# Kernel tuning notes

Hardware: AMD Instinct MI355X
Metric: run time of the kernel (lower is better)

Reference implementation:

```python
import jax, jax.numpy as jnp
import numpy as np

L, B, T, C, H, FC = 8, 4, 2048, 1024, 16, 4
HD = C // H  # head dim = 64
DFF = FC * C  # 4096


def _layernorm(x, g, b, eps=1e-5):
    mu = jnp.mean(x, axis=-1, keepdims=True)
    var = jnp.mean(jnp.square(x - mu), axis=-1, keepdims=True)
    return (x - mu) * jax.lax.rsqrt(var + eps) * g + b


def setup_inputs() -> dict:
    key = jax.random.key(0)
    ks = jax.random.split(key, 18)
    s = 0.02
    d = {}
    d["x"] = jax.random.normal(ks[0], (B, T, C), jnp.float32)
    d["ln1_g"] = jnp.ones((L, C), jnp.float32)
    d["ln1_b"] = jnp.zeros((L, C), jnp.float32)
    d["ln2_g"] = jnp.ones((L, C), jnp.float32)
    d["ln2_b"] = jnp.zeros((L, C), jnp.float32)
    d["wq"] = jax.random.normal(ks[1], (L, C, C), jnp.float32) * s
    d["bq"] = jnp.zeros((L, C), jnp.float32)
    d["wk"] = jax.random.normal(ks[2], (L, C, C), jnp.float32) * s
    d["bk"] = jnp.zeros((L, C), jnp.float32)
    d["wv"] = jax.random.normal(ks[3], (L, C, C), jnp.float32) * s
    d["bv"] = jnp.zeros((L, C), jnp.float32)
    d["wo"] = jax.random.normal(ks[4], (L, C, C), jnp.float32) * s
    d["bo"] = jnp.zeros((L, C), jnp.float32)
    d["w1"] = jax.random.normal(ks[5], (L, C, DFF), jnp.float32) * s
    d["b1"] = jnp.zeros((L, DFF), jnp.float32)
    d["w2"] = jax.random.normal(ks[6], (L, DFF, C), jnp.float32) * s
    d["b2"] = jnp.zeros((L, C), jnp.float32)
    return d


def _forward(x, ln1_g, ln1_b, ln2_g, ln2_b, wq, bq, wk, bk, wv, bv, wo, bo, w1, b1, w2, b2):
    mask = jnp.tril(jnp.ones((T, T), dtype=bool))  # causal mask (block_size buffer)
    scale = 1.0 / np.sqrt(HD).astype(np.float32)

    def block(h, p):
        g1, be1, g2, be2, Wq, Bq, Wk, Bk, Wv, Bv, Wo, Bo, W1, B1, W2, B2 = p
        hn = _layernorm(h, g1, be1)
        # heads: [B, H, T, HD]
        q = (hn @ Wq + Bq).reshape(B, T, H, HD).transpose(0, 2, 1, 3)
        k = (hn @ Wk + Bk).reshape(B, T, H, HD).transpose(0, 2, 1, 3)
        v = (hn @ Wv + Bv).reshape(B, T, H, HD).transpose(0, 2, 1, 3)
        att = jnp.einsum('bhid,bhjd->bhij', q, k) * scale
        att = jnp.where(mask, att, -jnp.inf)
        att = jax.nn.softmax(att, axis=-1)
        y = jnp.einsum('bhij,bhjd->bhid', att, v)
        y = y.transpose(0, 2, 1, 3).reshape(B, T, C) @ Wo + Bo
        h = h + y
        m = _layernorm(h, g2, be2)
        h = h + jax.nn.gelu(m @ W1 + B1, approximate=False) @ W2 + B2
        return h, None

    params = (ln1_g, ln1_b, ln2_g, ln2_b, wq, bq, wk, bk, wv, bv, wo, bo, w1, b1, w2, b2)
    x, _ = jax.lax.scan(block, x, params)
    return x


def reference(x, ln1_g, ln1_b, ln2_g, ln2_b, wq, bq, wk, bk, wv, bv, wo, bo, w1, b1, w2, b2):
    return _forward(x, ln1_g, ln1_b, ln2_g, ln2_b, wq, bq, wk, bk, wv, bv, wo, bo, w1, b1, w2, b2)
```

## Files before the change

kernel.cpp:

```cpp
#include <hip/hip_runtime.h>
#include <hip/hip_bf16.h>

#define LL 8
#define BBx 4
#define TT 2048
#define CC 1024
#define HH 16
#define HDD 64
#define DFFx 4096
#define MMx 8192

typedef __bf16 bf16;
typedef __attribute__((ext_vector_type(8))) __bf16 bf16x8;
typedef __attribute__((ext_vector_type(4))) __bf16 bf16x4;
typedef __attribute__((ext_vector_type(4))) float f32x4;
typedef __attribute__((ext_vector_type(8))) unsigned short u16x8;

__device__ __forceinline__ unsigned short bfbits(float v) {
  return __builtin_bit_cast(unsigned short, (__bf16)v);
}

__device__ __forceinline__ int xcd_swz(int id, int nwg) {
  return (id & 7) * (nwg >> 3) + (id >> 3);
}

#define GLDS(gp, lp) __builtin_amdgcn_global_load_lds( \
    (const __attribute__((address_space(1))) void*)(gp), \
    (__attribute__((address_space(3))) void*)(lp), 16, 0, 0)

__global__ __launch_bounds__(256) void transpose_cast(
    const float* __restrict__ W, bf16* __restrict__ Wt,
    int K, int N, long srcStride, long dstStride)
{
  __shared__ float tile[32][33];
  const float* Wl = W + (size_t)blockIdx.z * srcStride;
  bf16* Wtl = Wt + (size_t)blockIdx.z * dstStride;
  const int n0 = blockIdx.x * 32, k0 = blockIdx.y * 32;
  const int tx = threadIdx.x, ty = threadIdx.y;
#pragma unroll
  for (int i = 0; i < 32; i += 8)
    tile[ty + i][tx] = Wl[(size_t)(k0 + ty + i) * N + n0 + tx];
  __syncthreads();
#pragma unroll
  for (int i = 0; i < 32; i += 8)
    Wtl[(size_t)(n0 + ty + i) * K + k0 + tx] = (bf16)tile[tx][ty + i];
}

__global__ __launch_bounds__(256) void ln_cmb(
    float* __restrict__ h, const float* __restrict__ p0, const float* __restrict__ p1,
    const float* __restrict__ gamma, const float* __restrict__ beta,
    bf16* __restrict__ out)
{
  const int row = blockIdx.x, tid = threadIdx.x;
  const size_t base = (size_t)row * CC + tid * 4;
  float4 v = *(const float4*)(h + base);
  if (p0) {
    const float4 a = *(const float4*)(p0 + base);
    const float4 b = *(const float4*)(p1 + base);
    v.x += a.x + b.x; v.y += a.y + b.y; v.z += a.z + b.z; v.w += a.w + b.w;
    *(float4*)(h + base) = v;
  }
  if (!out) return;
  float s  = v.x + v.y + v.z + v.w;
  float ss = v.x * v.x + v.y * v.y + v.z * v.z + v.w * v.w;
#pragma unroll
  for (int o = 32; o >= 1; o >>= 1) {
    s  += __shfl_xor(s, o);
    ss += __shfl_xor(ss, o);
  }
  __shared__ float rs[4], rss[4];
  const int w = tid >> 6, l = tid & 63;
  if (l == 0) { rs[w] = s; rss[w] = ss; }
  __syncthreads();
  s  = rs[0] + rs[1] + rs[2] + rs[3];
  ss = rss[0] + rss[1] + rss[2] + rss[3];
  const float mu = s * (1.f / CC);
  const float rstd = rsqrtf(ss * (1.f / CC) - mu * mu + 1e-5f);
  const float4 g  = *(const float4*)(gamma + tid * 4);
  const float4 be = *(const float4*)(beta + tid * 4);
  bf16x4 o4;
  o4[0] = (bf16)((v.x - mu) * rstd * g.x + be.x);
  o4[1] = (bf16)((v.y - mu) * rstd * g.y + be.y);
  o4[2] = (bf16)((v.z - mu) * rstd * g.z + be.z);
  o4[3] = (bf16)((v.w - mu) * rstd * g.w + be.w);
  *(bf16x4*)(out + (size_t)row * CC + tid * 4) = o4;
}

template<int EPI>
__global__ __launch_bounds__(512, 2) void gemm256(
    const bf16* __restrict__ A, const bf16* __restrict__ Bt,
    const float* __restrict__ bias0, const float* __restrict__ bias1,
    const float* __restrict__ bias2,
    bf16* __restrict__ o0, bf16* __restrict__ o1, bf16* __restrict__ o2,
    float* __restrict__ p0, float* __restrict__ p1,
    int M, int N, int K, int lda)
{
  __shared__ __align__(16) bf16 sA[2][256 * 64];
  __shared__ __align__(16) bf16 sB[2][256 * 64];
  const int nx = N >> 8;
  int wk = xcd_swz((int)blockIdx.x, (int)gridDim.x);
  int koff = 0;
  float* part = p0;
  bool addb = true;
  if constexpr (EPI == 1) {
    const int tiles = nx * (M >> 8);
    const int ks = wk / tiles;
    wk -= ks * tiles;
    koff = ks * K;
    addb = (ks == 0);
    part = ks ? p1 : p0;
  }
  const int m0 = (wk / nx) * 256;
  const int n0 = (wk % nx) * 256;
  const int tid = threadIdx.x;
  const int w = tid >> 6, l = tid & 63;
  const int wm = w >> 2, wn = w & 3;
  const int lr = l & 15, lk = l >> 4;
  const int sr = tid >> 3, ss = tid & 7;

  f32x4 acc[8][4] = {};
  const int NT = K >> 6;

  auto stage = [&](int b, int kt) {
    const int gc = ((ss ^ (sr & 7)) << 3) + kt * 64 + koff;
#pragma unroll
    for (int i = 0; i < 4; ++i) {
      const int r = sr + i * 64;
      const int dst = r * 64 + ss * 8;
      GLDS(A + (size_t)(m0 + r) * lda + gc, &sA[b][dst]);
      GLDS(Bt + (size_t)(n0 + r) * lda + gc, &sB[b][dst]);
    }
  };

  stage(0, 0);
  int cur = 0;
  for (int kt = 0; kt < NT; ++kt) {
    if (kt + 1 < NT) {
      stage(cur ^ 1, kt + 1);
      asm volatile("s_waitcnt vmcnt(8)" ::: "memory");
    } else {
      asm volatile("s_waitcnt vmcnt(0)" ::: "memory");
    }
    __builtin_amdgcn_s_barrier();
#pragma unroll
    for (int kk = 0; kk < 2; ++kk) {
      bf16x8 af[8], bfr[4];
#pragma unroll
      for (int m = 0; m < 8; ++m) {
        const int row = wm * 128 + m * 16 + lr;
        af[m] = *(const bf16x8*)&sA[cur][row * 64 + (((kk * 4 + lk) ^ (row & 7)) << 3)];
      }
#pragma unroll
      for (int j = 0; j < 4; ++j) {
        const int row = wn * 64 + j * 16 + lr;
        bfr[j] = *(const bf16x8*)&sB[cur][row * 64 + (((kk * 4 + lk) ^ (row & 7)) << 3)];
      }
#pragma unroll
      for (int m = 0; m < 8; ++m)
#pragma unroll
        for (int j = 0; j < 4; ++j)
          acc[m][j] = __builtin_amdgcn_mfma_f32_16x16x32_bf16(af[m], bfr[j], acc[m][j], 0, 0, 0);
    }
    __builtin_amdgcn_s_barrier();
    cur ^= 1;
  }

  if constexpr (EPI == 0) {
    const int seg = n0 >> 10;
    const float* bp = (seg == 0) ? bias0 : (seg == 1 ? bias1 : bias2);
    if (seg < 2) {
      float bv4[4];
#pragma unroll
      for (int j = 0; j < 4; ++j) bv4[j] = bp[(n0 + wn * 64 + j * 16 + lr) & 1023];
      const int hh = ((n0 + wn * 64) & 1023) >> 6;
      bf16* dst = (seg == 0) ? o0 : o1;
#pragma unroll
      for (int m = 0; m < 8; ++m) {
        const int mrow = m0 + wm * 128 + m * 16 + lk * 4;
        const int bidx = mrow >> 11, t = mrow & 2047;
#pragma unroll
        for (int r = 0; r < 4; ++r) {
          bf16* rowp = dst + (((size_t)(bidx * HH + hh)) * TT + t + r) * HDD;
#pragma unroll
          for (int j = 0; j < 4; ++j)
            rowp[j * 16 + lr] = (bf16)(acc[m][j][r] + bv4[j]);
        }
      }
    } else {
      char* scb = (char*)((w < 4) ? (&sA[0][0] + w * 8192) : (&sB[0][0] + (w - 4) * 8192));
#pragma unroll
      for (int j = 0; j < 4; ++j) {
        const int dl = j * 16 + lr;
        const float bv = bias2[(n0 + wn * 64 + dl) & 1023];
#pragma unroll
        for (int m = 0; m < 8; ++m) {
          ushort4 pk;
          pk.x = bfbits(acc[m][j][0] + bv);
          pk.y = bfbits(acc[m][j][1] + bv);
          pk.z = bfbits(acc[m][j][2] + bv);
          pk.w = bfbits(acc[m][j][3] + bv);
          *(ushort4*)(scb + dl * 256 + (((m * 16 + lk * 4) * 2) ^ ((dl & 7) << 4))) = pk;
        }
      }
      asm volatile("s_waitcnt lgkmcnt(0)" ::: "memory");
      const int hh = ((n0 + wn * 64) & 1023) >> 6;
      const int bidx = m0 >> 11;
      const int tb = ((m0 + wm * 128) & 2047);
      const int c = l & 15;
#pragma unroll
      for (int g = 0; g < 16; ++g) {
        const int dl = g * 4 + lk;
        u16x8 val = *(const u16x8*)(scb + dl * 256 + ((c * 16) ^ ((dl & 7) << 4)));
        *(u16x8*)&o2[(((size_t)(bidx * HH + hh)) * HDD + dl) * TT + tb + c * 8] = val;
      }
    }
  } else if constexpr (EPI == 1) {
    float bv4[4];
#pragma unroll
    for (int j = 0; j < 4; ++j)
      bv4[j] = addb ? bias0[n0 + wn * 64 + j * 16 + lr] : 0.f;
#pragma unroll
    for (int m = 0; m < 8; ++m) {
      const int mrow = m0 + wm * 128 + m * 16 + lk * 4;
#pragma unroll
      for (int r = 0; r < 4; ++r) {
        float* rowp = part + (size_t)(mrow + r) * N + n0 + wn * 64;
#pragma unroll
        for (int j = 0; j < 4; ++j)
          rowp[j * 16 + lr] = acc[m][j][r] + bv4[j];
      }
    }
  } else {
    float bv4[4];
#pragma unroll
    for (int j = 0; j < 4; ++j) bv4[j] = bias0[n0 + wn * 64 + j * 16 + lr];
#pragma unroll
    for (int m = 0; m < 8; ++m) {
      const int mrow = m0 + wm * 128 + m * 16 + lk * 4;
#pragma unroll
      for (int r = 0; r < 4; ++r) {
        bf16* rowp = o0 + (size_t)(mrow + r) * N + n0 + wn * 64;
#pragma unroll
        for (int j = 0; j < 4; ++j) {
          const float x = acc[m][j][r] + bv4[j];
          rowp[j * 16 + lr] = (bf16)(0.5f * x * (1.f + erff(x * 0.70710678f)));
        }
      }
    }
  }
  (void)M;
}

__global__ __launch_bounds__(256) void attn_fwd(
    const bf16* __restrict__ Q, const bf16* __restrict__ Kk,
    const bf16* __restrict__ Vt, bf16* __restrict__ O)
{
  const int wk = xcd_swz((int)blockIdx.x, (int)gridDim.x);
  const int bh = wk >> 3;
  const int xt = wk & 7;
  const int tid = threadIdx.x;
  const int w = tid >> 6, l = tid & 63;
  const int lr = l & 15, lk = l >> 4;
  const int bidx = bh >> 4, hh = bh & 15;

  const bf16* Qp = Q  + (size_t)bh * (TT * HDD);
  const bf16* Kp = Kk + (size_t)bh * (TT * HDD);
  const bf16* Vp = Vt + (size_t)bh * (HDD * TT);

  __shared__ __align__(16) bf16 sK[64 * 64];
  __shared__ __align__(16) bf16 sV[64 * 64];
  __shared__ __align__(16) bf16 sP[4][16 * 64];
  bf16* sPw = &sP[w][0];

  const float sc = 0.125f;
  const int swz = (lr & 7) * 8;
  const int srow = tid >> 3;
  const int scol = (((tid & 7) ^ (srow & 7)) << 3);
  const int sdst = tid << 3;

  for (int half = 0; half < 2; ++half) {
    const int qtile = (half == 0) ? xt : (15 - xt);
    const int q0 = qtile * 128;

    bf16x8 qf[2][2];
#pragma unroll
    for (int qi = 0; qi < 2; ++qi)
#pragma unroll
      for (int dk = 0; dk < 2; ++dk)
        qf[qi][dk] = *(const bf16x8*)&Qp[(size_t)(q0 + w * 32 + qi * 16 + lr) * HDD + dk * 32 + lk * 8];

    f32x4 accO[2][4] = {};
    float mrun[2] = {-__builtin_inff(), -__builtin_inff()};
    float lrun[2] = {0.f, 0.f};
    const int wqmax = q0 + w * 32 + 31;
    const int kvend = q0 + 128;

    for (int kv = 0; kv < kvend; kv += 64) {
      __syncthreads();
#pragma unroll
      for (int i = 0; i < 2; ++i) {
        GLDS(Kp + (size_t)(kv + srow + i * 32) * HDD + scol, sK + sdst + i * 2048);
        GLDS(Vp + (size_t)(srow + i * 32) * TT + kv + scol, sV + sdst + i * 2048);
      }
      __syncthreads();

      if (kv <= wqmax) {
#pragma unroll
        for (int qi = 0; qi < 2; ++qi) {
          f32x4 st[4];
#pragma unroll
          for (int kt = 0; kt < 4; ++kt) {
            f32x4 z = {0.f, 0.f, 0.f, 0.f};
#pragma unroll
            for (int dk = 0; dk < 2; ++dk) {
              bf16x8 kf = *(const bf16x8*)&sK[(kt * 16 + lr) * 64 + ((dk * 32 + lk * 8) ^ swz)];
              z = __builtin_amdgcn_mfma_f32_16x16x32_bf16(kf, qf[qi][dk], z, 0, 0, 0);
            }
            st[kt] = z;
          }
          const int qabs = q0 + w * 32 + qi * 16 + lr;
          float pm = -__builtin_inff();
#pragma unroll
          for (int kt = 0; kt < 4; ++kt)
#pragma unroll
            for (int r = 0; r < 4; ++r) {
              const int kvabs = kv + kt * 16 + lk * 4 + r;
              float val = st[kt][r] * sc;
              val = (kvabs > qabs) ? -__builtin_inff() : val;
              st[kt][r] = val;
              pm = fmaxf(pm, val);
            }
          pm = fmaxf(pm, __shfl_xor(pm, 16));
          pm = fmaxf(pm, __shfl_xor(pm, 32));
          const float mnew = fmaxf(mrun[qi], pm);
          const float alpha = __expf(mrun[qi] - mnew);
          mrun[qi] = mnew;
          float psum = 0.f;
#pragma unroll
          for (int kt = 0; kt < 4; ++kt) {
            const float p0v = __expf(st[kt][0] - mnew);
            const float p1v = __expf(st[kt][1] - mnew);
            const float p2v = __expf(st[kt][2] - mnew);
            const float p3v = __expf(st[kt][3] - mnew);
            psum += p0v + p1v + p2v + p3v;
            ushort4 pk;
            pk.x = bfbits(p0v); pk.y = bfbits(p1v); pk.z = bfbits(p2v); pk.w = bfbits(p3v);
            *(ushort4*)&sPw[lr * 64 + ((kt * 16 + lk * 4) ^ swz)] = pk;
          }
          psum += __shfl_xor(psum, 16);
          psum += __shfl_xor(psum, 32);
          lrun[qi] = lrun[qi] * alpha + psum;
          f32x4 al4;
#pragma unroll
          for (int r = 0; r < 4; ++r) al4[r] = __shfl(alpha, lk * 4 + r);
#pragma unroll
          for (int dj = 0; dj < 4; ++dj) accO[qi][dj] *= al4;
#pragma unroll
          for (int kt2 = 0; kt2 < 2; ++kt2) {
            bf16x8 pf = *(const bf16x8*)&sPw[lr * 64 + ((kt2 * 32 + lk * 8) ^ swz)];
#pragma unroll
            for (int dj = 0; dj < 4; ++dj) {
              bf16x8 vf = *(const bf16x8*)&sV[(dj * 16 + lr) * 64 + ((kt2 * 32 + lk * 8) ^ swz)];
              accO[qi][dj] = __builtin_amdgcn_mfma_f32_16x16x32_bf16(pf, vf, accO[qi][dj], 0, 0, 0);
            }
          }
        }
      }
    }

#pragma unroll
    for (int qi = 0; qi < 2; ++qi) {
      const float linv = 1.f / lrun[qi];
      f32x4 li4;
#pragma unroll
      for (int r = 0; r < 4; ++r) li4[r] = __shfl(linv, lk * 4 + r);
      const int tbase = q0 + w * 32 + qi * 16 + lk * 4;
#pragma unroll
      for (int dj = 0; dj < 4; ++dj)
#pragma unroll
        for (int r = 0; r < 4; ++r)
          O[((size_t)bidx * TT + tbase + r) * CC + hh * 64 + dj * 16 + lr] =
              (bf16)(accO[qi][dj][r] * li4[r]);
    }
  }
}

extern "C" void kernel_launch(void* const* d_in, const int* in_sizes, int n_in,
                              void* d_out, int out_size, void* d_ws, size_t ws_size,
                              hipStream_t stream)
{
  const float* x    = (const float*)d_in[0];
  const float* ln1g = (const float*)d_in[1];
  const float* ln1b = (const float*)d_in[2];
  const float* ln2g = (const float*)d_in[3];
  const float* ln2b = (const float*)d_in[4];
  const float* wq   = (const float*)d_in[5];
  const float* bq   = (const float*)d_in[6];
  const float* wk   = (const float*)d_in[7];
  const float* bk   = (const float*)d_in[8];
  const float* wv   = (const float*)d_in[9];
  const float* bvv  = (const float*)d_in[10];
  const float* wo   = (const float*)d_in[11];
  const float* bo   = (const float*)d_in[12];
  const float* w1   = (const float*)d_in[13];
  const float* b1   = (const float*)d_in[14];
  const float* w2   = (const float*)d_in[15];
  const float* b2   = (const float*)d_in[16];

  float* h = (float*)d_out;
  bf16* ws = (bf16*)d_ws;
  bf16* wqkvT = ws;
  bf16* woT   = wqkvT + (size_t)LL * 3 * CC * CC;
  bf16* w1T   = woT + (size_t)LL * CC * CC;
  bf16* w2T   = w1T + (size_t)LL * CC * DFFx;
  bf16* hn    = w2T + (size_t)LL * CC * DFFx;
  bf16* qb    = hn + (size_t)MMx * CC;
  bf16* kb    = qb + (size_t)MMx * CC;
  bf16* vt    = kb + (size_t)MMx * CC;
  bf16* ab    = vt + (size_t)MMx * CC;
  bf16* mid   = ab + (size_t)MMx * CC;

  float* pw0 = (float*)mid;
  float* pw1 = (float*)mid + (size_t)MMx * CC;
  float* pm0 = (float*)qb;
  float* pm1 = (float*)vt;

  hipMemcpyAsync(h, x, (size_t)MMx * CC * sizeof(float), hipMemcpyDeviceToDevice, stream);

  dim3 tb(32, 8);
  transpose_cast<<<dim3(CC / 32, CC / 32, LL), tb, 0, stream>>>(wq, wqkvT, CC, CC, (long)CC * CC, (long)3 * CC * CC);
  transpose_cast<<<dim3(CC / 32, CC / 32, LL), tb, 0, stream>>>(wk, wqkvT + CC * CC, CC, CC, (long)CC * CC, (long)3 * CC * CC);
  transpose_cast<<<dim3(CC / 32, CC / 32, LL), tb, 0, stream>>>(wv, wqkvT + 2 * CC * CC, CC, CC, (long)CC * CC, (long)3 * CC * CC);
  transpose_cast<<<dim3(CC / 32, CC / 32, LL), tb, 0, stream>>>(wo, woT, CC, CC, (long)CC * CC, (long)CC * CC);
  transpose_cast<<<dim3(DFFx / 32, CC / 32, LL), tb, 0, stream>>>(w1, w1T, CC, DFFx, (long)CC * DFFx, (long)CC * DFFx);
  transpose_cast<<<dim3(CC / 32, DFFx / 32, LL), tb, 0, stream>>>(w2, w2T, DFFx, CC, (long)CC * DFFx, (long)CC * DFFx);

  for (int li = 0; li < LL; ++li) {
    if (li == 0)
      ln_cmb<<<MMx, 256, 0, stream>>>(h, nullptr, nullptr, ln1g, ln1b, hn);
    else
      ln_cmb<<<MMx, 256, 0, stream>>>(h, pm0, pm1, ln1g + li * CC, ln1b + li * CC, hn);
    gemm256<0><<<(3 * CC / 256) * (MMx / 256), 512, 0, stream>>>(
        hn, wqkvT + (size_t)li * 3 * CC * CC, bq + li * CC, bk + li * CC, bvv + li * CC,
        qb, kb, vt, nullptr, nullptr, MMx, 3 * CC, CC, CC);
    attn_fwd<<<8 * BBx * HH, 256, 0, stream>>>(qb, kb, vt, ab);
    gemm256<1><<<2 * (CC / 256) * (MMx / 256), 512, 0, stream>>>(
        ab, woT + (size_t)li * CC * CC, bo + li * CC, nullptr, nullptr,
        nullptr, nullptr, nullptr, pw0, pw1, MMx, CC, CC / 2, CC);
    ln_cmb<<<MMx, 256, 0, stream>>>(h, pw0, pw1, ln2g + li * CC, ln2b + li * CC, hn);
    gemm256<2><<<(DFFx / 256) * (MMx / 256), 512, 0, stream>>>(
        hn, w1T + (size_t)li * CC * DFFx, b1 + li * DFFx, nullptr, nullptr,
        mid, nullptr, nullptr, nullptr, nullptr, MMx, DFFx, CC, CC);
    gemm256<1><<<2 * (CC / 256) * (MMx / 256), 512, 0, stream>>>(
        mid, w2T + (size_t)li * CC * DFFx, b2 + li * CC, nullptr, nullptr,
        nullptr, nullptr, nullptr, pm0, pm1, MMx, CC, DFFx / 2, DFFx);
  }
  ln_cmb<<<MMx, 256, 0, stream>>>(h, pm0, pm1, nullptr, nullptr, nullptr);
  (void)in_sizes; (void)n_in; (void)out_size; (void)ws_size;
}
```

Before: 3.480 ms.

## Replace 256x256 double-buffered GEMM with 128x128 single-buffered tile kernel

Shrinks the GEMM block tile from 256x256 with 512 threads to 128x128 with 256 threads, raising the occupancy hint and the grid size. It also drops LDS double buffering and the XOR swizzle on shared-memory reads, loading each K tile synchronously before compute. The intent is likely more blocks for better load balance and occupancy. The cost is lost load/compute overlap, lower reuse per tile, and possible LDS bank conflicts.

```diff
diff --git a/kernel.cpp b/kernel.cpp
--- a/kernel.cpp
+++ b/kernel.cpp
@@ -87,7 +87,7 @@
 }
 
 template<int EPI>
-__global__ __launch_bounds__(512, 2) void gemm256(
+__global__ __launch_bounds__(256, 4) void gemm128(
     const bf16* __restrict__ A, const bf16* __restrict__ Bt,
     const float* __restrict__ bias0, const float* __restrict__ bias1,
     const float* __restrict__ bias2,
@@ -95,74 +95,56 @@
     float* __restrict__ p0, float* __restrict__ p1,
     int M, int N, int K, int lda)
 {
-  __shared__ __align__(16) bf16 sA[2][256 * 64];
-  __shared__ __align__(16) bf16 sB[2][256 * 64];
-  const int nx = N >> 8;
+  __shared__ __align__(16) bf16 sA[128 * 64];
+  __shared__ __align__(16) bf16 sB[128 * 64];
+  const int nx = N >> 7;
   int wk = xcd_swz((int)blockIdx.x, (int)gridDim.x);
   int koff = 0;
   float* part = p0;
   bool addb = true;
   if constexpr (EPI == 1) {
-    const int tiles = nx * (M >> 8);
+    const int tiles = nx * (M >> 7);
     const int ks = wk / tiles;
     wk -= ks * tiles;
     koff = ks * K;
     addb = (ks == 0);
     part = ks ? p1 : p0;
   }
-  const int m0 = (wk / nx) * 256;
-  const int n0 = (wk % nx) * 256;
+  const int m0 = (wk / nx) * 128;
+  const int n0 = (wk % nx) * 128;
   const int tid = threadIdx.x;
   const int w = tid >> 6, l = tid & 63;
-  const int wm = w >> 2, wn = w & 3;
+  const int wr = w >> 1, wc = w & 1;
   const int lr = l & 15, lk = l >> 4;
-  const int sr = tid >> 3, ss = tid & 7;
-
-  f32x4 acc[8][4] = {};
+
+  f32x4 acc[4][4] = {};
   const int NT = K >> 6;
 
-  auto stage = [&](int b, int kt) {
-    const int gc = ((ss ^ (sr & 7)) << 3) + kt * 64 + koff;
+  for (int kt = 0; kt < NT; ++kt) {
 #pragma unroll
     for (int i = 0; i < 4; ++i) {
-      const int r = sr + i * 64;
-      const int dst = r * 64 + ss * 8;
-      GLDS(A + (size_t)(m0 + r) * lda + gc, &sA[b][dst]);
-      GLDS(Bt + (size_t)(n0 + r) * lda + gc, &sB[b][dst]);
-    }
-  };
-
-  stage(0, 0);
-  int cur = 0;
-  for (int kt = 0; kt < NT; ++kt) {
-    if (kt + 1 < NT) {
-      stage(cur ^ 1, kt + 1);
-      asm volatile("s_waitcnt vmcnt(8)" ::: "memory");
-    } else {
-      asm volatile("s_waitcnt vmcnt(0)" ::: "memory");
-    }
-    __builtin_amdgcn_s_barrier();
+      const int e = (tid << 4) + (i << 12);
+      const int ro = e >> 7, co = (e & 127) >> 1;
+      GLDS(A + (size_t)(m0 + ro) * lda + kt * 64 + koff + co, sA + (e >> 1));
+      GLDS(Bt + (size_t)(n0 + ro) * lda + kt * 64 + koff + co, sB + (e >> 1));
+    }
+    __syncthreads();
 #pragma unroll
     for (int kk = 0; kk < 2; ++kk) {
-      bf16x8 af[8], bfr[4];
-#pragma unroll
-      for (int m = 0; m < 8; ++m) {
-        const int row = wm * 128 + m * 16 + lr;
-        af[m] = *(const bf16x8*)&sA[cur][row * 64 + (((kk * 4 + lk) ^ (row & 7)) << 3)];
-      }
-#pragma unroll
-      for (int j = 0; j < 4; ++j) {
-        const int row = wn * 64 + j * 16 + lr;
-        bfr[j] = *(const bf16x8*)&sB[cur][row * 64 + (((kk * 4 + lk) ^ (row & 7)) << 3)];
-      }
-#pragma unroll
-      for (int m = 0; m < 8; ++m)
+      bf16x8 af[4], bfr[4];
+#pragma unroll
+      for (int i = 0; i < 4; ++i)
+        af[i] = *(const bf16x8*)&sA[(wr * 64 + i * 16 + lr) * 64 + kk * 32 + lk * 8];
+#pragma unroll
+      for (int j = 0; j < 4; ++j)
+        bfr[j] = *(const bf16x8*)&sB[(wc * 64 + j * 16 + lr) * 64 + kk * 32 + lk * 8];
+#pragma unroll
+      for (int i = 0; i < 4; ++i)
 #pragma unroll
         for (int j = 0; j < 4; ++j)
-          acc[m][j] = __builtin_amdgcn_mfma_f32_16x16x32_bf16(af[m], bfr[j], acc[m][j], 0, 0, 0);
-    }
-    __builtin_amdgcn_s_barrier();
-    cur ^= 1;
+          acc[i][j] = __builtin_amdgcn_mfma_f32_16x16x32_bf16(af[i], bfr[j], acc[i][j], 0, 0, 0);
+    }
+    __syncthreads();
   }
 
   if constexpr (EPI == 0) {
@@ -171,46 +153,46 @@
     if (seg < 2) {
       float bv4[4];
 #pragma unroll
-      for (int j = 0; j < 4; ++j) bv4[j] = bp[(n0 + wn * 64 + j * 16 + lr) & 1023];
-      const int hh = ((n0 + wn * 64) & 1023) >> 6;
+      for (int j = 0; j < 4; ++j) bv4[j] = bp[(n0 + wc * 64 + j * 16 + lr) & 1023];
+      const int hh = ((n0 + wc * 64) & 1023) >> 6;
       bf16* dst = (seg == 0) ? o0 : o1;
 #pragma unroll
-      for (int m = 0; m < 8; ++m) {
-        const int mrow = m0 + wm * 128 + m * 16 + lk * 4;
+      for (int i = 0; i < 4; ++i) {
+        const int mrow = m0 + wr * 64 + i * 16 + lk * 4;
         const int bidx = mrow >> 11, t = mrow & 2047;
 #pragma unroll
         for (int r = 0; r < 4; ++r) {
           bf16* rowp = dst + (((size_t)(bidx * HH + hh)) * TT + t + r) * HDD;
 #pragma unroll
           for (int j = 0; j < 4; ++j)
-            rowp[j * 16 + lr] = (bf16)(acc[m][j][r] + bv4[j]);
+            rowp[j * 16 + lr] = (bf16)(acc[i][j][r] + bv4[j]);
         }
       }
     } else {
-      char* scb = (char*)((w < 4) ? (&sA[0][0] + w * 8192) : (&sB[0][0] + (w - 4) * 8192));
+      char* scb = (w < 2) ? ((char*)sA + w * 8192) : ((char*)sB + (w - 2) * 8192);
 #pragma unroll
       for (int j = 0; j < 4; ++j) {
         const int dl = j * 16 + lr;
-        const float bv = bias2[(n0 + wn * 64 + dl) & 1023];
-#pragma unroll
-        for (int m = 0; m < 8; ++m) {
+        const float bv = bias2[(n0 + wc * 64 + dl) & 1023];
+#pragma unroll
+        for (int i = 0; i < 4; ++i) {
           ushort4 pk;
-          pk.x = bfbits(acc[m][j][0] + bv);
-          pk.y = bfbits(acc[m][j][1] + bv);
-          pk.z = bfbits(acc[m][j][2] + bv);
-          pk.w = bfbits(acc[m][j][3] + bv);
-          *(ushort4*)(scb + dl * 256 + (((m * 16 + lk * 4) * 2) ^ ((dl & 7) << 4))) = pk;
+          pk.x = bfbits(acc[i][j][0] + bv);
+          pk.y = bfbits(acc[i][j][1] + bv);
+          pk.z = bfbits(acc[i][j][2] + bv);
+          pk.w = bfbits(acc[i][j][3] + bv);
+          *(ushort4*)(scb + dl * 128 + (((i * 16 + lk * 4) * 2) ^ ((dl & 7) << 4))) = pk;
         }
       }
       asm volatile("s_waitcnt lgkmcnt(0)" ::: "memory");
-      const int hh = ((n0 + wn * 64) & 1023) >> 6;
-      const int bidx = m0 >> 11;
-      const int tb = ((m0 + wm * 128) & 2047);
-      const int c = l & 15;
-#pragma unroll
-      for (int g = 0; g < 16; ++g) {
-        const int dl = g * 4 + lk;
-        u16x8 val = *(const u16x8*)(scb + dl * 256 + ((c * 16) ^ ((dl & 7) << 4)));
+      const int hh = ((n0 + wc * 64) & 1023) >> 6;
+      const int bidx = (m0 + wr * 64) >> 11;
+      const int tb = (m0 + wr * 64) & 2047;
+      const int c = l & 7;
+#pragma unroll
+      for (int g = 0; g < 8; ++g) {
+        const int dl = g * 8 + (l >> 3);
+        u16x8 val = *(const u16x8*)(scb + dl * 128 + ((c * 16) ^ ((dl & 7) << 4)));
         *(u16x8*)&o2[(((size_t)(bidx * HH + hh)) * HDD + dl) * TT + tb + c * 8] = val;
       }
     }
@@ -218,31 +200,31 @@
     float bv4[4];
 #pragma unroll
     for (int j = 0; j < 4; ++j)
-      bv4[j] = addb ? bias0[n0 + wn * 64 + j * 16 + lr] : 0.f;
-#pragma unroll
-    for (int m = 0; m < 8; ++m) {
-      const int mrow = m0 + wm * 128 + m * 16 + lk * 4;
+      bv4[j] = addb ? bias0[n0 + wc * 64 + j * 16 + lr] : 0.f;
+#pragma unroll
+    for (int i = 0; i < 4; ++i) {
+      const int mrow = m0 + wr * 64 + i * 16 + lk * 4;
 #pragma unroll
       for (int r = 0; r < 4; ++r) {
-        float* rowp = part + (size_t)(mrow + r) * N + n0 + wn * 64;
+        float* rowp = part + (size_t)(mrow + r) * N + n0 + wc * 64;
 #pragma unroll
         for (int j = 0; j < 4; ++j)
-          rowp[j * 16 + lr] = acc[m][j][r] + bv4[j];
+          rowp[j * 16 + lr] = acc[i][j][r] + bv4[j];
       }
     }
   } else {
     float bv4[4];
 #pragma unroll
-    for (int j = 0; j < 4; ++j) bv4[j] = bias0[n0 + wn * 64 + j * 16 + lr];
-#pragma unroll
-    for (int m = 0; m < 8; ++m) {
-      const int mrow = m0 + wm * 128 + m * 16 + lk * 4;
+    for (int j = 0; j < 4; ++j) bv4[j] = bias0[n0 + wc * 64 + j * 16 + lr];
+#pragma unroll
+    for (int i = 0; i < 4; ++i) {
+      const int mrow = m0 + wr * 64 + i * 16 + lk * 4;
 #pragma unroll
       for (int r = 0; r < 4; ++r) {
-        bf16* rowp = o0 + (size_t)(mrow + r) * N + n0 + wn * 64;
+        bf16* rowp = o0 + (size_t)(mrow + r) * N + n0 + wc * 64;
 #pragma unroll
         for (int j = 0; j < 4; ++j) {
-          const float x = acc[m][j][r] + bv4[j];
+          const float x = acc[i][j][r] + bv4[j];
           rowp[j * 16 + lr] = (bf16)(0.5f * x * (1.f + erff(x * 0.70710678f)));
         }
       }
@@ -440,18 +422,18 @@
       ln_cmb<<<MMx, 256, 0, stream>>>(h, nullptr, nullptr, ln1g, ln1b, hn);
     else
       ln_cmb<<<MMx, 256, 0, stream>>>(h, pm0, pm1, ln1g + li * CC, ln1b + li * CC, hn);
-    gemm256<0><<<(3 * CC / 256) * (MMx / 256), 512, 0, stream>>>(
+    gemm128<0><<<(3 * CC / 128) * (MMx / 128), 256, 0, stream>>>(
         hn, wqkvT + (size_t)li * 3 * CC * CC, bq + li * CC, bk + li * CC, bvv + li * CC,
         qb, kb, vt, nullptr, nullptr, MMx, 3 * CC, CC, CC);
     attn_fwd<<<8 * BBx * HH, 256, 0, stream>>>(qb, kb, vt, ab);
-    gemm256<1><<<2 * (CC / 256) * (MMx / 256), 512, 0, stream>>>(
+    gemm128<1><<<2 * (CC / 128) * (MMx / 128), 256, 0, stream>>>(
         ab, woT + (size_t)li * CC * CC, bo + li * CC, nullptr, nullptr,
         nullptr, nullptr, nullptr, pw0, pw1, MMx, CC, CC / 2, CC);
     ln_cmb<<<MMx, 256, 0, stream>>>(h, pw0, pw1, ln2g + li * CC, ln2b + li * CC, hn);
-    gemm256<2><<<(DFFx / 256) * (MMx / 256), 512, 0, stream>>>(
+    gemm128<2><<<(DFFx / 128) * (MMx / 128), 256, 0, stream>>>(
         hn, w1T + (size_t)li * CC * DFFx, b1 + li * DFFx, nullptr, nullptr,
         mid, nullptr, nullptr, nullptr, nullptr, MMx, DFFx, CC, CC);
-    gemm256<1><<<2 * (CC / 256) * (MMx / 256), 512, 0, stream>>>(
+    gemm128<1><<<2 * (CC / 128) * (MMx / 128), 256, 0, stream>>>(
         mid, w2T + (size_t)li * CC * DFFx, b2 + li * CC, nullptr, nullptr,
         nullptr, nullptr, nullptr, pm0, pm1, MMx, CC, DFFx / 2, DFFx);
   }
```

Measured after the change: 3.320 ms. 4.6% less time.
